# Kernel tuning notes

Hardware: AMD Instinct MI355X
Metric: run time of the kernel (lower is better)

## Reference

```python
import jax, jax.numpy as jnp
import numpy as np

PH = 32          # prediction horizon (unroll steps)
HID = 512        # hidden_dim == latent_dim (output fed back as input)
OUT = 2          # output_dim
BS = 2048


def setup_inputs() -> dict:
    key = jax.random.key(0)
    ks = jax.random.split(key, 8)
    s = 1.0 / np.sqrt(HID)
    return {
        "hist": jax.random.normal(ks[0], (BS, 8, 2), dtype=jnp.float32),
        "z": jax.random.normal(ks[1], (BS, 1, HID), dtype=jnp.float32),
        # LSTMCell params (PyTorch layout: [4H, in], gate order i,f,g,o)
        "W_ih": jax.random.uniform(ks[2], (4 * HID, HID), jnp.float32, -s, s),
        "W_hh": jax.random.uniform(ks[3], (4 * HID, HID), jnp.float32, -s, s),
        "b_ih": jax.random.uniform(ks[4], (4 * HID,), jnp.float32, -s, s),
        "b_hh": jax.random.uniform(ks[5], (4 * HID,), jnp.float32, -s, s),
        # dense: hidden_dim -> output_dim
        "W_d": jax.random.uniform(ks[6], (OUT, HID), jnp.float32, -s, s),
        "b_d": jax.random.uniform(ks[7], (OUT,), jnp.float32, -s, s),
    }


def reference(hist, z, W_ih, W_hh, b_ih, b_hh, W_d, b_d):
    bs = z.shape[0]
    x0 = z.reshape(bs, -1)                       # [bs, H]
    h0 = jnp.zeros((bs, HID), dtype=z.dtype)
    c0 = jnp.zeros((bs, HID), dtype=z.dtype)

    def step(carry, _):
        x, h, c = carry
        gates = x @ W_ih.T + b_ih + h @ W_hh.T + b_hh   # [bs, 4H]
        i, f, g, o = jnp.split(gates, 4, axis=-1)
        c_new = jax.nn.sigmoid(f) * c + jax.nn.sigmoid(i) * jnp.tanh(g)
        h_new = jax.nn.sigmoid(o) * jnp.tanh(c_new)
        # output h is fed back as next input
        return (h_new, h_new, c_new), h_new

    _, hs = jax.lax.scan(step, (x0, h0, c0), None, length=PH)  # [PH, bs, H]
    out_all = jnp.swapaxes(hs, 0, 1)                           # [bs, PH, H]
    y = out_all @ W_d.T + b_d                                  # [bs, PH, OUT]
    return y
```

## Files before the change

kernel.cpp:

```cpp
#include <hip/hip_runtime.h>
#include <hip/hip_bf16.h>

#define BS_   2048
#define HID_  512
#define PH_   32
#define GRP_  16

typedef _Float16 half8 __attribute__((ext_vector_type(8)));
typedef float floatx4 __attribute__((ext_vector_type(4)));

__device__ __forceinline__ float sigf(float x) { return 1.f / (1.f + __expf(-x)); }
__device__ __forceinline__ float tanhfast(float x) {
    float e = __expf(2.f * x);
    return 1.f - 2.f / (e + 1.f);
}

__global__ __launch_bounds__(256) void prep_kernel(
    const float* __restrict__ Wih, const float* __restrict__ Whh,
    const float* __restrict__ bih, const float* __restrict__ bhh,
    const float* __restrict__ z,
    _Float16* __restrict__ wih16, _Float16* __restrict__ wsum16,
    _Float16* __restrict__ z16, float* __restrict__ bsum,
    int* __restrict__ cnt)
{
    int i = blockIdx.x * 256 + threadIdx.x;
    if (i < BS_ * HID_) z16[i] = (_Float16)z[i];
    if (i < 4 * HID_ * HID_) {
        float a = Wih[i];
        wih16[i]  = (_Float16)a;
        wsum16[i] = (_Float16)(a + Whh[i]);
    }
    if (i < 4 * HID_) bsum[i] = bih[i] + bhh[i];
    if (i < 512) cnt[i] = 0;
}

__device__ __forceinline__ void stage_weights(_Float16* Wl, const _Float16* Wg,
                                              int j, int tid)
{
#pragma unroll
    for (int rep = 0; rep < 16; ++rep) {
        int idx = rep * 512 + tid;
        int n  = idx >> 6;
        int kb = idx & 63;
        int g  = n >> 5, u = n & 31;
        const half8* src = (const half8*)(Wg + ((size_t)(g * HID_ + j * 32 + u)) * HID_ + kb * 8);
        int phys = (kb & 56) | ((kb & 7) ^ (n & 7));
        *(half8*)((char*)Wl + n * 1024 + phys * 16) = *src;
    }
}

__global__ __launch_bounds__(512) void lstm_persist(
    const _Float16* __restrict__ wih16, const _Float16* __restrict__ wsum16,
    const float* __restrict__ bsum, const _Float16* __restrict__ z16,
    _Float16* __restrict__ hs, int* __restrict__ cnt)
{
    __shared__ _Float16 Wl[128 * 512];

    const int tid  = threadIdx.x;
    const int ib   = blockIdx.x & 15;
    const int j    = blockIdx.x >> 4;
    const int lane = tid & 63;
    const int wv   = tid >> 6;
    const int ms   = wv & 3;
    const int hh   = wv >> 2;
    const int qw   = lane >> 4;
    const int ln   = lane & 15;
    const int hid  = j * 32 + hh * 16 + ln;

    stage_weights(Wl, wih16, j, tid);

    float bias[4];
#pragma unroll
    for (int g = 0; g < 4; ++g) bias[g] = bsum[g * HID_ + hid];

    float c[2][4];
#pragma unroll
    for (int mt = 0; mt < 2; ++mt)
#pragma unroll
        for (int r = 0; r < 4; ++r) c[mt][r] = 0.f;

    const char* Bl = (const char*)Wl;
    const int tE = (qw ^ (ln & 7)) * 16;
    const int rowB = hh * 16 + ln;

    __syncthreads();

    for (int t = 0; t < PH_; ++t) {
        const _Float16* xx = (t == 0) ? z16 : hs + (size_t)(t - 1) * BS_ * HID_;

        if (t >= 1) {
            if (tid == 0) {
                while (__hip_atomic_fetch_add(&cnt[ib * 32 + t - 1], 0,
                                              __ATOMIC_RELAXED,
                                              __HIP_MEMORY_SCOPE_AGENT) < GRP_) {
                    __builtin_amdgcn_s_sleep(1);
                }
            }
            __syncthreads();
        }

        floatx4 acc[2][4];
#pragma unroll
        for (int mt = 0; mt < 2; ++mt)
#pragma unroll
            for (int g = 0; g < 4; ++g)
                acc[mt][g] = (floatx4){bias[g], bias[g], bias[g], bias[g]};

        const _Float16* A0 = xx + (size_t)(ib * 128 + ms * 32 + ln) * HID_ + qw * 8;

        half8 a0r[4], a1r[4], bA[4], bB[4];
#pragma unroll
        for (int p = 0; p < 4; ++p) {
            a0r[p] = *(const half8*)(A0 + p * 32);
            a1r[p] = *(const half8*)(A0 + 16 * HID_ + p * 32);
        }
#pragma unroll
        for (int g = 0; g < 4; ++g)
            bA[g] = *(const half8*)(Bl + (g * 32 + rowB) * 1024 + tE);

#pragma unroll
        for (int kk = 0; kk < 16; ++kk) {
            half8 ca0 = a0r[kk & 3], ca1 = a1r[kk & 3];
            if (kk < 12) {
                a0r[kk & 3] = *(const half8*)(A0 + (kk + 4) * 32);
                a1r[kk & 3] = *(const half8*)(A0 + 16 * HID_ + (kk + 4) * 32);
            }
            half8* cb = (kk & 1) ? bB : bA;
            half8* nb = (kk & 1) ? bA : bB;
            if (kk < 15) {
                int k1 = kk + 1;
#pragma unroll
                for (int g = 0; g < 4; ++g) {
                    int off = (g * 32 + rowB) * 1024 + (k1 >> 1) * 128 + (tE ^ ((k1 & 1) << 6));
                    nb[g] = *(const half8*)(Bl + off);
                }
            }
#pragma unroll
            for (int g = 0; g < 4; ++g) {
                acc[0][g] = __builtin_amdgcn_mfma_f32_16x16x32_f16(ca0, cb[g], acc[0][g], 0, 0, 0);
                acc[1][g] = __builtin_amdgcn_mfma_f32_16x16x32_f16(ca1, cb[g], acc[1][g], 0, 0, 0);
            }
        }

        _Float16* hb = hs + (size_t)t * BS_ * HID_
                          + (size_t)(ib * 128 + ms * 32 + qw * 4) * HID_ + hid;
#pragma unroll
        for (int mt = 0; mt < 2; ++mt) {
#pragma unroll
            for (int r = 0; r < 4; ++r) {
                float gi = acc[mt][0][r];
                float gf = acc[mt][1][r];
                float gg = acc[mt][2][r];
                float go = acc[mt][3][r];
                float cn = sigf(gf) * c[mt][r] + sigf(gi) * tanhfast(gg);
                float hn = sigf(go) * tanhfast(cn);
                c[mt][r] = cn;
                _Float16 hf = (_Float16)hn;
                short hv;
                __builtin_memcpy(&hv, &hf, 2);
                __hip_atomic_store((short*)(hb + (size_t)(mt * 16 + r) * HID_), hv,
                                   __ATOMIC_RELAXED, __HIP_MEMORY_SCOPE_AGENT);
            }
        }

        __syncthreads();
        if (t == 0) {
            if (tid == 0)
                __hip_atomic_fetch_add(&cnt[ib * 32], 1,
                                       __ATOMIC_RELAXED, __HIP_MEMORY_SCOPE_AGENT);
            stage_weights(Wl, wsum16, j, tid);
            __syncthreads();
        } else if (t < PH_ - 1) {
            if (tid == 0)
                __hip_atomic_fetch_add(&cnt[ib * 32 + t], 1,
                                       __ATOMIC_RELAXED, __HIP_MEMORY_SCOPE_AGENT);
        }
    }
}

__global__ __launch_bounds__(256) void dense_kernel(
    const _Float16* __restrict__ hs, const float* __restrict__ Wd,
    const float* __restrict__ bd, float* __restrict__ y)
{
    int gw   = (blockIdx.x * 256 + threadIdx.x) >> 6;
    int lane = threadIdx.x & 63;
    int tt = gw & 31, b = gw >> 5;
    half8 h = *(const half8*)(hs + ((size_t)tt * BS_ + b) * HID_ + lane * 8);
    float s0 = 0.f, s1 = 0.f;
#pragma unroll
    for (int k = 0; k < 8; ++k) {
        float hv = (float)h[k];
        s0 += hv * Wd[lane * 8 + k];
        s1 += hv * Wd[HID_ + lane * 8 + k];
    }
#pragma unroll
    for (int m = 32; m >= 1; m >>= 1) {
        s0 += __shfl_xor(s0, m);
        s1 += __shfl_xor(s1, m);
    }
    if (lane == 0) {
        float* o = y + ((size_t)b * PH_ + tt) * 2;
        o[0] = s0 + bd[0];
        o[1] = s1 + bd[1];
    }
}

extern "C" void kernel_launch(void* const* d_in, const int* in_sizes, int n_in,
                              void* d_out, int out_size, void* d_ws, size_t ws_size,
                              hipStream_t stream)
{
    (void)in_sizes; (void)n_in; (void)out_size; (void)ws_size;
    const float* z   = (const float*)d_in[1];
    const float* Wih = (const float*)d_in[2];
    const float* Whh = (const float*)d_in[3];
    const float* bih = (const float*)d_in[4];
    const float* bhh = (const float*)d_in[5];
    const float* Wd  = (const float*)d_in[6];
    const float* bd  = (const float*)d_in[7];
    float* y = (float*)d_out;

    char* ws = (char*)d_ws;
    _Float16* hs     = (_Float16*)ws;
    _Float16* z16    = (_Float16*)(ws + (size_t)67108864);
    _Float16* wih16  = (_Float16*)(ws + (size_t)69206016);
    _Float16* wsum16 = (_Float16*)(ws + (size_t)71303168);
    float*    bsum   = (float*)   (ws + (size_t)73400320);
    int*      cnt    = (int*)     (ws + (size_t)73408512);

    prep_kernel<<<4096, 256, 0, stream>>>(Wih, Whh, bih, bhh, z,
                                          wih16, wsum16, z16, bsum, cnt);

    {
        const void* k = (const void*)lstm_persist;
        void* args[] = {(void*)&wih16, (void*)&wsum16, (void*)&bsum,
                        (void*)&z16, (void*)&hs, (void*)&cnt};
        hipLaunchCooperativeKernel(k, dim3(256), dim3(512), args, 0, stream);
    }

    dense_kernel<<<16384, 256, 0, stream>>>(hs, Wd, bd, y);
}
```

Baseline: 425.6 us.

## Fuse dense projection into LSTM kernel and use plain stores when group shares an XCD

The output projection moves into the persistent LSTM kernel. Each wave computes partial dot products of h with W_d through lane shuffles and writes per-slice partials, and a small reduce kernel then sums 32 partials per output. This replaces the dense kernel's re-read of all hidden states. The LSTM also records each block's XCD id in a bitmask, and when all blocks of a batch group sit on one XCD it writes h with ordinary stores instead of agent-scope atomic stores. The last step's h is no longer written. These changes add shuffle work and extra partial-result stores in the recurrent loop, and the fast path relies on coherence within a single XCD.

```diff
diff --git a/kernel.cpp b/kernel.cpp
--- a/kernel.cpp
+++ b/kernel.cpp
@@ -5,6 +5,8 @@
 #define HID_  512
 #define PH_   32
 #define GRP_  16
+
+#define HWREG_XCC_ID ((3 << 11) | (0 << 6) | 20)
 
 typedef _Float16 half8 __attribute__((ext_vector_type(8)));
 typedef float floatx4 __attribute__((ext_vector_type(4)));
@@ -31,7 +33,7 @@
         wsum16[i] = (_Float16)(a + Whh[i]);
     }
     if (i < 4 * HID_) bsum[i] = bih[i] + bhh[i];
-    if (i < 512) cnt[i] = 0;
+    if (i < 520) cnt[i] = 0;
 }
 
 __device__ __forceinline__ void stage_weights(_Float16* Wl, const _Float16* Wg,
@@ -52,9 +54,11 @@
 __global__ __launch_bounds__(512) void lstm_persist(
     const _Float16* __restrict__ wih16, const _Float16* __restrict__ wsum16,
     const float* __restrict__ bsum, const _Float16* __restrict__ z16,
-    _Float16* __restrict__ hs, int* __restrict__ cnt)
+    _Float16* __restrict__ hs, int* __restrict__ cnt,
+    const float* __restrict__ Wd, float* __restrict__ yp)
 {
     __shared__ _Float16 Wl[128 * 512];
+    __shared__ int sh_fast;
 
     const int tid  = threadIdx.x;
     const int ib   = blockIdx.x & 15;
@@ -72,6 +76,8 @@
     float bias[4];
 #pragma unroll
     for (int g = 0; g < 4; ++g) bias[g] = bsum[g * HID_ + hid];
+    const float wd0 = Wd[hid];
+    const float wd1 = Wd[HID_ + hid];
 
     float c[2][4];
 #pragma unroll
@@ -82,6 +88,9 @@
     const char* Bl = (const char*)Wl;
     const int tE = (qw ^ (ln & 7)) * 16;
     const int rowB = hh * 16 + ln;
+
+    bool fast = false;
+    int* xmask = cnt + 512;
 
     __syncthreads();
 
@@ -95,8 +104,15 @@
                                               __HIP_MEMORY_SCOPE_AGENT) < GRP_) {
                     __builtin_amdgcn_s_sleep(1);
                 }
+                if (t == 1) {
+                    int m = __hip_atomic_fetch_add(&xmask[ib], 0,
+                                                   __ATOMIC_RELAXED,
+                                                   __HIP_MEMORY_SCOPE_AGENT);
+                    sh_fast = (__popc((unsigned)m) == 1) ? 1 : 0;
+                }
             }
             __syncthreads();
+            if (t == 1) fast = (sh_fast != 0);
         }
 
         floatx4 acc[2][4];
@@ -144,6 +160,7 @@
 
         _Float16* hb = hs + (size_t)t * BS_ * HID_
                           + (size_t)(ib * 128 + ms * 32 + qw * 4) * HID_ + hid;
+        float* ypb = yp + ((size_t)(t * 32 + (j * 2 + hh)) * 2048) * 2;
 #pragma unroll
         for (int mt = 0; mt < 2; ++mt) {
 #pragma unroll
@@ -155,19 +172,41 @@
                 float cn = sigf(gf) * c[mt][r] + sigf(gi) * tanhfast(gg);
                 float hn = sigf(go) * tanhfast(cn);
                 c[mt][r] = cn;
-                _Float16 hf = (_Float16)hn;
-                short hv;
-                __builtin_memcpy(&hv, &hf, 2);
-                __hip_atomic_store((short*)(hb + (size_t)(mt * 16 + r) * HID_), hv,
-                                   __ATOMIC_RELAXED, __HIP_MEMORY_SCOPE_AGENT);
+
+                float p0 = hn * wd0, p1 = hn * wd1;
+#pragma unroll
+                for (int m = 1; m <= 8; m <<= 1) {
+                    p0 += __shfl_xor(p0, m);
+                    p1 += __shfl_xor(p1, m);
+                }
+                if (ln == 0) {
+                    int row = ib * 128 + ms * 32 + mt * 16 + qw * 4 + r;
+                    *(float2*)(ypb + (size_t)row * 2) = make_float2(p0, p1);
+                }
+
+                if (t < PH_ - 1) {
+                    if (fast) {
+                        hb[(size_t)(mt * 16 + r) * HID_] = (_Float16)hn;
+                    } else {
+                        _Float16 hf = (_Float16)hn;
+                        short hv;
+                        __builtin_memcpy(&hv, &hf, 2);
+                        __hip_atomic_store((short*)(hb + (size_t)(mt * 16 + r) * HID_), hv,
+                                           __ATOMIC_RELAXED, __HIP_MEMORY_SCOPE_AGENT);
+                    }
+                }
             }
         }
 
         __syncthreads();
         if (t == 0) {
-            if (tid == 0)
+            if (tid == 0) {
+                int xcd = __builtin_amdgcn_s_getreg(HWREG_XCC_ID) & 0xf;
+                __hip_atomic_fetch_or(&xmask[ib], 1 << xcd,
+                                      __ATOMIC_RELAXED, __HIP_MEMORY_SCOPE_AGENT);
                 __hip_atomic_fetch_add(&cnt[ib * 32], 1,
-                                       __ATOMIC_RELAXED, __HIP_MEMORY_SCOPE_AGENT);
+                                       __ATOMIC_RELEASE, __HIP_MEMORY_SCOPE_AGENT);
+            }
             stage_weights(Wl, wsum16, j, tid);
             __syncthreads();
         } else if (t < PH_ - 1) {
@@ -178,31 +217,20 @@
     }
 }
 
-__global__ __launch_bounds__(256) void dense_kernel(
-    const _Float16* __restrict__ hs, const float* __restrict__ Wd,
-    const float* __restrict__ bd, float* __restrict__ y)
-{
-    int gw   = (blockIdx.x * 256 + threadIdx.x) >> 6;
-    int lane = threadIdx.x & 63;
-    int tt = gw & 31, b = gw >> 5;
-    half8 h = *(const half8*)(hs + ((size_t)tt * BS_ + b) * HID_ + lane * 8);
-    float s0 = 0.f, s1 = 0.f;
-#pragma unroll
-    for (int k = 0; k < 8; ++k) {
-        float hv = (float)h[k];
-        s0 += hv * Wd[lane * 8 + k];
-        s1 += hv * Wd[HID_ + lane * 8 + k];
-    }
-#pragma unroll
-    for (int m = 32; m >= 1; m >>= 1) {
-        s0 += __shfl_xor(s0, m);
-        s1 += __shfl_xor(s1, m);
-    }
-    if (lane == 0) {
-        float* o = y + ((size_t)b * PH_ + tt) * 2;
-        o[0] = s0 + bd[0];
-        o[1] = s1 + bd[1];
-    }
+__global__ __launch_bounds__(256) void reduce_kernel(
+    const float* __restrict__ yp, const float* __restrict__ bd,
+    float* __restrict__ y)
+{
+    int gw = blockIdx.x * 256 + threadIdx.x;
+    int b = gw & 2047, t = gw >> 11;
+    float s0 = bd[0], s1 = bd[1];
+#pragma unroll 4
+    for (int s = 0; s < 32; ++s) {
+        float2 v = *(const float2*)(yp + ((size_t)(t * 32 + s) * 2048 + b) * 2);
+        s0 += v.x; s1 += v.y;
+    }
+    float* o = y + ((size_t)b * PH_ + t) * 2;
+    o[0] = s0; o[1] = s1;
 }
 
 extern "C" void kernel_launch(void* const* d_in, const int* in_sizes, int n_in,
@@ -226,6 +254,7 @@
     _Float16* wsum16 = (_Float16*)(ws + (size_t)71303168);
     float*    bsum   = (float*)   (ws + (size_t)73400320);
     int*      cnt    = (int*)     (ws + (size_t)73408512);
+    float*    yp     = (float*)   (ws + (size_t)73412608);
 
     prep_kernel<<<4096, 256, 0, stream>>>(Wih, Whh, bih, bhh, z,
                                           wih16, wsum16, z16, bsum, cnt);
@@ -233,9 +262,10 @@
     {
         const void* k = (const void*)lstm_persist;
         void* args[] = {(void*)&wih16, (void*)&wsum16, (void*)&bsum,
-                        (void*)&z16, (void*)&hs, (void*)&cnt};
+                        (void*)&z16, (void*)&hs, (void*)&cnt,
+                        (void*)&Wd, (void*)&yp};
         hipLaunchCooperativeKernel(k, dim3(256), dim3(512), args, 0, stream);
     }
 
-    dense_kernel<<<16384, 256, 0, stream>>>(hs, Wd, bd, y);
-}
+    reduce_kernel<<<256, 256, 0, stream>>>(yp, bd, y);
+}
```

Result: slower. 479.1 us (+12.6%).
